# Kernel optimization log

Hardware: AMD Instinct MI355X
Metric: run time of the kernel (lower is better)

## Reference

```python
import jax, jax.numpy as jnp
import numpy as np

TEMPERATURE = 10.0  # module init temperature (training mode)


def setup_inputs() -> dict:
    key = jax.random.key(0)
    kx, kg = jax.random.split(key)
    B, C, H, W = 64, 128, 64, 64
    n = C * H * W  # 524288
    x = jax.random.normal(kx, (B, C, H, W), dtype=jnp.float32)
    # Gumbel(0,1) noise for Gumbel-top-k sampling (== multinomial w/o replacement)
    u = jax.random.uniform(kg, (B, n), dtype=jnp.float32, minval=1e-20, maxval=1.0)
    gumbel = -jnp.log(-jnp.log(u))
    k = int(round(0.1 * n))  # percent_on * n = 52429
    return {"x": x, "gumbel": gumbel, "k": k}


def reference(x, gumbel, k):
    B = x.shape[0]
    n = x.shape[1] * x.shape[2] * x.shape[3]
    flat = x.reshape(B, n)                      # [B, n]
    logits = flat / TEMPERATURE
    # Categorical sampling of k winners without replacement == top-k of
    # gumbel-perturbed logits (equivalent to softmax(logits) + multinomial).
    _, idx = jax.lax.top_k(logits + gumbel, k)  # [B, k]
    mask = jnp.zeros((B, n), dtype=x.dtype).at[jnp.arange(B)[:, None], idx].set(1.0)
    out = (flat * mask).reshape(x.shape)
    return jnp.maximum(out, 0.0)  # relu=True
```

## Files before the change

kernel.cpp:

```cpp
#include <hip/hip_runtime.h>
#include <cstdint>

#define BROWS 64
#define NCOL  524288
#define CHUNKS 64
#define CHUNK  (NCOL / CHUNKS)
#define NV4    (CHUNK / 4)
#define LCAP   1024
#define ECAP   512
#define MAXCAP 24576
#define M_SAMP 32768
#define SEGS   128
#define SBLK   16
#define SLACK  5200
#define HB2    32768

typedef float nf4 __attribute__((ext_vector_type(4)));

#define ABV_OFF   0u
#define CCNT_OFF  256u
#define RINFO_OFF 512u
#define HIST_OFF  4096u
#define CAND_OFF  4096u
#define ZWORDS    (1024 + BROWS * HB2)

__device__ __forceinline__ uint32_t fkey(float s) {
  uint32_t b = __float_as_uint(s);
  return (b & 0x80000000u) ? ~b : (b | 0x80000000u);
}

__global__ __launch_bounds__(256) void k_zero(uint32_t* __restrict__ p, int n) {
  int i = blockIdx.x * 256 + threadIdx.x;
  if (i < n) p[i] = 0;
}

__global__ __launch_bounds__(256) void k_sampleA(const float* __restrict__ x,
                                                 const float* __restrict__ g,
                                                 uint32_t* __restrict__ hist) {
  int row = blockIdx.y;
  size_t rb = (size_t)row * NCOL;
  uint32_t* gh = hist + (size_t)row * HB2;
  int i0 = blockIdx.x * (M_SAMP / SBLK);
  for (int it = 0; it < (M_SAMP / SBLK) / 256; ++it) {
    int i = i0 + it * 256 + threadIdx.x;
    size_t off = rb + (size_t)(i >> 8) * (NCOL / SEGS) + (i & 255);
    uint32_t key = fkey(x[off] / 10.0f + g[off]);
    atomicAdd(&gh[key >> 17], 1u);
  }
}

__global__ __launch_bounds__(1024) void k_pick(const uint32_t* __restrict__ hist,
                                               const int* __restrict__ kptr,
                                               uint32_t* __restrict__ rinfo,
                                               uint32_t* __restrict__ abv,
                                               uint32_t* __restrict__ ccnt) {
  __shared__ uint32_t part[1024];
  __shared__ uint32_t segbuf[32];
  __shared__ uint32_t sel[4];
  int row = blockIdx.x;
  if (threadIdx.x == 0) { abv[row] = 0; ccnt[row] = 0; }
  const uint32_t* gh = hist + (size_t)row * HB2;
  const uint4* gh4 = (const uint4*)gh;
  uint32_t s = 0;
  #pragma unroll
  for (int j = 0; j < 8; ++j) {
    uint4 v = gh4[threadIdx.x * 8 + j];
    s += v.x + v.y + v.z + v.w;
  }
  part[threadIdx.x] = s;
  __syncthreads();
  if (threadIdx.x == 0) {
    uint32_t kk = (uint32_t)(*kptr);
    uint32_t rHi = ((kk > SLACK ? kk - SLACK : 0u) / 16u) + 1u;
    uint32_t rLo = ((kk + SLACK) / 16u) + 1u;
    if (rLo > M_SAMP) rLo = M_SAMP;
    uint32_t cum = 0, cumHi = 0, cumLo = 0;
    int segHi = -1, segLo = -1;
    for (int t = 1023; t >= 0; --t) {
      uint32_t c = part[t];
      if (segHi < 0 && cum + c >= rHi) { segHi = t; cumHi = cum; }
      if (segLo < 0 && cum + c >= rLo) { segLo = t; cumLo = cum; break; }
      cum += c;
    }
    if (segHi < 0) segHi = 0;
    if (segLo < 0) segLo = 0;
    sel[0] = (uint32_t)segHi; sel[1] = rHi - cumHi;
    sel[2] = (uint32_t)segLo; sel[3] = rLo - cumLo;
  }
  __syncthreads();
  int segHi = (int)sel[0], segLo = (int)sel[2];
  if (threadIdx.x < 32) segbuf[threadIdx.x] = gh[segHi * 32 + threadIdx.x];
  __syncthreads();
  if (threadIdx.x == 0) {
    uint32_t rem = sel[1], cum = 0;
    int bin = 0;
    for (int b = 31; b >= 0; --b) {
      uint32_t c = segbuf[b];
      if (cum + c >= rem) { bin = b; break; }
      cum += c;
    }
    uint32_t binHi = (uint32_t)(segHi * 32 + bin);
    rinfo[row * 4 + 0] = (binHi << 17) | 0x1FFFFu;
  }
  __syncthreads();
  if (threadIdx.x < 32) segbuf[threadIdx.x] = gh[segLo * 32 + threadIdx.x];
  __syncthreads();
  if (threadIdx.x == 0) {
    uint32_t rem = sel[3], cum = 0;
    int bin = 0;
    for (int b = 31; b >= 0; --b) {
      uint32_t c = segbuf[b];
      if (cum + c >= rem) { bin = b; break; }
      cum += c;
    }
    uint32_t binLo = (uint32_t)(segLo * 32 + bin);
    rinfo[row * 4 + 1] = binLo << 17;
  }
}

__global__ __launch_bounds__(256) void k_main(const float* __restrict__ x,
                                              const float* __restrict__ g,
                                              const uint32_t* __restrict__ rinfo,
                                              uint64_t* __restrict__ cand,
                                              float* __restrict__ cval,
                                              uint32_t* __restrict__ ccnt,
                                              uint32_t* __restrict__ abv,
                                              float* __restrict__ out, int cap) {
  __shared__ uint64_t lbuf[LCAP];
  __shared__ float lval[LCAP];
  __shared__ uint32_t lcnt, lbase;
  __shared__ uint32_t wsum[4];
  int row = blockIdx.y, chunk = blockIdx.x;
  uint32_t keyHi = rinfo[row * 4 + 0];
  uint32_t keyLo = rinfo[row * 4 + 1];
  if (threadIdx.x == 0) lcnt = 0;
  __syncthreads();
  size_t base = (size_t)row * NCOL + (size_t)chunk * CHUNK;
  const float4* x4 = (const float4*)(x + base);
  const float4* g4 = (const float4*)(g + base);
  nf4* o4 = (nf4*)(out + base);
  uint32_t mycnt = 0;
  for (int i = threadIdx.x; i < NV4; i += 256) {
    float4 a = x4[i];
    float4 b = g4[i];
    uint32_t f0 = fkey(a.x / 10.0f + b.x);
    uint32_t f1 = fkey(a.y / 10.0f + b.y);
    uint32_t f2 = fkey(a.z / 10.0f + b.z);
    uint32_t f3 = fkey(a.w / 10.0f + b.w);
    nf4 o;
    o.x = (f0 > keyHi) ? fmaxf(a.x, 0.0f) : 0.0f;
    o.y = (f1 > keyHi) ? fmaxf(a.y, 0.0f) : 0.0f;
    o.z = (f2 > keyHi) ? fmaxf(a.z, 0.0f) : 0.0f;
    o.w = (f3 > keyHi) ? fmaxf(a.w, 0.0f) : 0.0f;
    __builtin_nontemporal_store(o, &o4[i]);
    mycnt += (f0 > keyHi) + (f1 > keyHi) + (f2 > keyHi) + (f3 > keyHi);
    uint32_t li = (uint32_t)(chunk * CHUNK + i * 4);
    if (f0 >= keyLo && f0 <= keyHi) { uint32_t p = atomicAdd(&lcnt, 1u); if (p < LCAP) { lbuf[p] = ((uint64_t)f0 << 32) | li;        lval[p] = fmaxf(a.x, 0.0f); } }
    if (f1 >= keyLo && f1 <= keyHi) { uint32_t p = atomicAdd(&lcnt, 1u); if (p < LCAP) { lbuf[p] = ((uint64_t)f1 << 32) | (li + 1u); lval[p] = fmaxf(a.y, 0.0f); } }
    if (f2 >= keyLo && f2 <= keyHi) { uint32_t p = atomicAdd(&lcnt, 1u); if (p < LCAP) { lbuf[p] = ((uint64_t)f2 << 32) | (li + 2u); lval[p] = fmaxf(a.z, 0.0f); } }
    if (f3 >= keyLo && f3 <= keyHi) { uint32_t p = atomicAdd(&lcnt, 1u); if (p < LCAP) { lbuf[p] = ((uint64_t)f3 << 32) | (li + 3u); lval[p] = fmaxf(a.w, 0.0f); } }
  }
  for (int off = 32; off > 0; off >>= 1) mycnt += __shfl_down(mycnt, off);
  int lane = threadIdx.x & 63, wid = threadIdx.x >> 6;
  if (lane == 0) wsum[wid] = mycnt;
  __syncthreads();
  if (threadIdx.x == 0) {
    atomicAdd(&abv[row], wsum[0] + wsum[1] + wsum[2] + wsum[3]);
    lbase = atomicAdd(&ccnt[row], lcnt < LCAP ? lcnt : (uint32_t)LCAP);
  }
  __syncthreads();
  uint32_t cnt = lcnt < LCAP ? lcnt : (uint32_t)LCAP;
  uint64_t* dst = cand + (size_t)row * (size_t)cap;
  float* dv = cval + (size_t)row * (size_t)cap;
  for (uint32_t i = threadIdx.x; i < cnt; i += 256) {
    uint32_t p = lbase + i;
    if (p < (uint32_t)cap) { dst[p] = lbuf[i]; dv[p] = lval[i]; }
  }
}

__global__ __launch_bounds__(256) void k_finalize(const float* __restrict__ x,
                                                  const uint64_t* __restrict__ cand,
                                                  const float* __restrict__ cval,
                                                  const uint32_t* __restrict__ ccnt,
                                                  const uint32_t* __restrict__ abv,
                                                  const uint32_t* __restrict__ rinfo,
                                                  const int* __restrict__ kptr,
                                                  float* __restrict__ out, int cap) {
  __shared__ uint32_t h[4096];
  __shared__ uint32_t part[256];
  __shared__ uint64_t elist[ECAP];
  __shared__ uint32_t ecnt;
  __shared__ int s_cut, s_need2;
  int row = blockIdx.x;
  uint32_t m = ccnt[row];
  if (m > (uint32_t)cap) m = (uint32_t)cap;
  int need = (int)((uint32_t)(*kptr)) - (int)abv[row];
  if (need <= 0) return;
  size_t rb = (size_t)row * NCOL;
  const uint64_t* c = cand + (size_t)row * (size_t)cap;
  const float* cv = cval + (size_t)row * (size_t)cap;
  if ((uint32_t)need >= m) {
    for (uint32_t i = threadIdx.x; i < m; i += 256) {
      uint32_t idx = (uint32_t)c[i];
      out[rb + idx] = cv[i];
    }
    return;
  }
  uint32_t keyLo = rinfo[row * 4 + 1];
  uint32_t range = rinfo[row * 4 + 0] - keyLo;
  int bits = 32 - __clz((int)(range | 1u));
  int shift = bits > 12 ? bits - 12 : 0;
  for (int i = threadIdx.x; i < 4096; i += 256) h[i] = 0;
  if (threadIdx.x == 0) ecnt = 0;
  __syncthreads();
  for (uint32_t i = threadIdx.x; i < m; i += 256) {
    uint32_t key = (uint32_t)(c[i] >> 32);
    atomicAdd(&h[(key - keyLo) >> shift], 1u);
  }
  __syncthreads();
  uint32_t s = 0;
  for (int j = 0; j < 16; ++j) s += h[threadIdx.x * 16 + j];
  part[threadIdx.x] = s;
  __syncthreads();
  if (threadIdx.x == 0) {
    uint32_t cum = 0;
    int seg = 255;
    for (; seg > 0; --seg) {
      if (cum + part[seg] >= (uint32_t)need) break;
      cum += part[seg];
    }
    int bin = seg * 16 + 15;
    for (; bin > seg * 16; --bin) {
      if (cum + h[bin] >= (uint32_t)need) break;
      cum += h[bin];
    }
    s_cut = bin;
    s_need2 = need - (int)cum;
  }
  __syncthreads();
  int cut = s_cut, need2 = s_need2;
  for (uint32_t i = threadIdx.x; i < m; i += 256) {
    uint64_t e = c[i];
    int bin = (int)(((uint32_t)(e >> 32) - keyLo) >> shift);
    if (bin > cut) {
      out[rb + (uint32_t)e] = cv[i];
    } else if (bin == cut) {
      uint32_t p = atomicAdd(&ecnt, 1u);
      if (p < ECAP) elist[p] = e ^ 0xFFFFFFFFull;
    }
  }
  __syncthreads();
  int mm = (int)(ecnt < (uint32_t)ECAP ? ecnt : (uint32_t)ECAP);
  for (int pass = 0; pass < mm; ++pass) {
    for (int i = threadIdx.x; 2 * i + (pass & 1) + 1 < mm; i += 256) {
      int a2 = 2 * i + (pass & 1);
      uint64_t va = elist[a2], vb = elist[a2 + 1];
      if (vb > va) { elist[a2] = vb; elist[a2 + 1] = va; }
    }
    __syncthreads();
  }
  int w = need2 < mm ? need2 : mm;
  for (int i = threadIdx.x; i < w; i += 256) {
    uint32_t idx = ~(uint32_t)elist[i];
    out[rb + idx] = fmaxf(x[rb + idx], 0.0f);
  }
}

extern "C" void kernel_launch(void* const* d_in, const int* in_sizes, int n_in,
                              void* d_out, int out_size, void* d_ws, size_t ws_size,
                              hipStream_t stream) {
  const float* x = (const float*)d_in[0];
  const float* g = (const float*)d_in[1];
  const int* kptr = (const int*)d_in[2];
  float* out = (float*)d_out;
  char* ws = (char*)d_ws;

  uint32_t* abv = (uint32_t*)(ws + ABV_OFF);
  uint32_t* ccnt = (uint32_t*)(ws + CCNT_OFF);
  uint32_t* rinfo = (uint32_t*)(ws + RINFO_OFF);
  uint32_t* hist = (uint32_t*)(ws + HIST_OFF);
  uint64_t* cand = (uint64_t*)(ws + CAND_OFF);

  long cap_avail = ((long)ws_size - (long)CAND_OFF) / (12 * BROWS);
  int cap = cap_avail < MAXCAP ? (int)cap_avail : MAXCAP;
  if (cap < 1) cap = 1;
  float* cval = (float*)(ws + CAND_OFF + (size_t)BROWS * (size_t)cap * 8u);

  k_zero<<<(ZWORDS + 255) / 256, 256, 0, stream>>>((uint32_t*)ws, ZWORDS);
  dim3 sgrid(SBLK, BROWS);
  k_sampleA<<<sgrid, 256, 0, stream>>>(x, g, hist);
  k_pick<<<BROWS, 1024, 0, stream>>>(hist, kptr, rinfo, abv, ccnt);
  dim3 grid(CHUNKS, BROWS);
  k_main<<<grid, 256, 0, stream>>>(x, g, rinfo, cand, cval, ccnt, abv, out, cap);
  k_finalize<<<BROWS, 256, 0, stream>>>(x, cand, cval, ccnt, abv, rinfo, kptr, out, cap);
}
```

Before: 214.5 us.

## Coarsen sample histogram, batch candidate atomics, split finalize into cut and scatter

The sample histogram drops from 32768 to 16384 bins per row, so there is less to zero and scan, and it uses twice as many sample blocks. Candidate appends in the main pass now take one shared atomic per float4 group instead of one per element. The old per-row finalize kernel is split in two: a 64-block cut kernel picks the boundary bin and handles ties, and a separate 16x64-block scatter kernel writes the candidates above the cut, giving more parallelism for the scattered writes. The trade-offs are an extra kernel launch and a wider candidate key window, which could leave more candidates per row.

```diff
diff --git a/kernel.cpp b/kernel.cpp
--- a/kernel.cpp
+++ b/kernel.cpp
@@ -11,9 +11,10 @@
 #define MAXCAP 24576
 #define M_SAMP 32768
 #define SEGS   128
-#define SBLK   16
+#define SBLK   32
 #define SLACK  5200
-#define HB2    32768
+#define HB2    16384
+#define NSCAT  16
 
 typedef float nf4 __attribute__((ext_vector_type(4)));
 
@@ -45,7 +46,7 @@
     int i = i0 + it * 256 + threadIdx.x;
     size_t off = rb + (size_t)(i >> 8) * (NCOL / SEGS) + (i & 255);
     uint32_t key = fkey(x[off] / 10.0f + g[off]);
-    atomicAdd(&gh[key >> 17], 1u);
+    atomicAdd(&gh[key >> 18], 1u);
   }
 }
 
@@ -55,7 +56,7 @@
                                                uint32_t* __restrict__ abv,
                                                uint32_t* __restrict__ ccnt) {
   __shared__ uint32_t part[1024];
-  __shared__ uint32_t segbuf[32];
+  __shared__ uint32_t segbuf[16];
   __shared__ uint32_t sel[4];
   int row = blockIdx.x;
   if (threadIdx.x == 0) { abv[row] = 0; ccnt[row] = 0; }
@@ -63,8 +64,8 @@
   const uint4* gh4 = (const uint4*)gh;
   uint32_t s = 0;
   #pragma unroll
-  for (int j = 0; j < 8; ++j) {
-    uint4 v = gh4[threadIdx.x * 8 + j];
+  for (int j = 0; j < 4; ++j) {
+    uint4 v = gh4[threadIdx.x * 4 + j];
     s += v.x + v.y + v.z + v.w;
   }
   part[threadIdx.x] = s;
@@ -89,32 +90,32 @@
   }
   __syncthreads();
   int segHi = (int)sel[0], segLo = (int)sel[2];
-  if (threadIdx.x < 32) segbuf[threadIdx.x] = gh[segHi * 32 + threadIdx.x];
+  if (threadIdx.x < 16) segbuf[threadIdx.x] = gh[segHi * 16 + threadIdx.x];
   __syncthreads();
   if (threadIdx.x == 0) {
     uint32_t rem = sel[1], cum = 0;
     int bin = 0;
-    for (int b = 31; b >= 0; --b) {
+    for (int b = 15; b >= 0; --b) {
       uint32_t c = segbuf[b];
       if (cum + c >= rem) { bin = b; break; }
       cum += c;
     }
-    uint32_t binHi = (uint32_t)(segHi * 32 + bin);
-    rinfo[row * 4 + 0] = (binHi << 17) | 0x1FFFFu;
-  }
-  __syncthreads();
-  if (threadIdx.x < 32) segbuf[threadIdx.x] = gh[segLo * 32 + threadIdx.x];
+    uint32_t binHi = (uint32_t)(segHi * 16 + bin);
+    rinfo[row * 4 + 0] = (binHi << 18) | 0x3FFFFu;
+  }
+  __syncthreads();
+  if (threadIdx.x < 16) segbuf[threadIdx.x] = gh[segLo * 16 + threadIdx.x];
   __syncthreads();
   if (threadIdx.x == 0) {
     uint32_t rem = sel[3], cum = 0;
     int bin = 0;
-    for (int b = 31; b >= 0; --b) {
+    for (int b = 15; b >= 0; --b) {
       uint32_t c = segbuf[b];
       if (cum + c >= rem) { bin = b; break; }
       cum += c;
     }
-    uint32_t binLo = (uint32_t)(segLo * 32 + bin);
-    rinfo[row * 4 + 1] = binLo << 17;
+    uint32_t binLo = (uint32_t)(segLo * 16 + bin);
+    rinfo[row * 4 + 1] = binLo << 18;
   }
 }
 
@@ -154,11 +155,19 @@
     o.w = (f3 > keyHi) ? fmaxf(a.w, 0.0f) : 0.0f;
     __builtin_nontemporal_store(o, &o4[i]);
     mycnt += (f0 > keyHi) + (f1 > keyHi) + (f2 > keyHi) + (f3 > keyHi);
-    uint32_t li = (uint32_t)(chunk * CHUNK + i * 4);
-    if (f0 >= keyLo && f0 <= keyHi) { uint32_t p = atomicAdd(&lcnt, 1u); if (p < LCAP) { lbuf[p] = ((uint64_t)f0 << 32) | li;        lval[p] = fmaxf(a.x, 0.0f); } }
-    if (f1 >= keyLo && f1 <= keyHi) { uint32_t p = atomicAdd(&lcnt, 1u); if (p < LCAP) { lbuf[p] = ((uint64_t)f1 << 32) | (li + 1u); lval[p] = fmaxf(a.y, 0.0f); } }
-    if (f2 >= keyLo && f2 <= keyHi) { uint32_t p = atomicAdd(&lcnt, 1u); if (p < LCAP) { lbuf[p] = ((uint64_t)f2 << 32) | (li + 2u); lval[p] = fmaxf(a.z, 0.0f); } }
-    if (f3 >= keyLo && f3 <= keyHi) { uint32_t p = atomicAdd(&lcnt, 1u); if (p < LCAP) { lbuf[p] = ((uint64_t)f3 << 32) | (li + 3u); lval[p] = fmaxf(a.w, 0.0f); } }
+    bool c0 = (f0 >= keyLo) && (f0 <= keyHi);
+    bool c1 = (f1 >= keyLo) && (f1 <= keyHi);
+    bool c2 = (f2 >= keyLo) && (f2 <= keyHi);
+    bool c3 = (f3 >= keyLo) && (f3 <= keyHi);
+    uint32_t nh = (uint32_t)c0 + (uint32_t)c1 + (uint32_t)c2 + (uint32_t)c3;
+    if (nh) {
+      uint32_t li = (uint32_t)(chunk * CHUNK + i * 4);
+      uint32_t p = atomicAdd(&lcnt, nh);
+      if (c0) { if (p < LCAP) { lbuf[p] = ((uint64_t)f0 << 32) | li;        lval[p] = fmaxf(a.x, 0.0f); } p++; }
+      if (c1) { if (p < LCAP) { lbuf[p] = ((uint64_t)f1 << 32) | (li + 1u); lval[p] = fmaxf(a.y, 0.0f); } p++; }
+      if (c2) { if (p < LCAP) { lbuf[p] = ((uint64_t)f2 << 32) | (li + 2u); lval[p] = fmaxf(a.z, 0.0f); } p++; }
+      if (c3) { if (p < LCAP) { lbuf[p] = ((uint64_t)f3 << 32) | (li + 3u); lval[p] = fmaxf(a.w, 0.0f); } p++; }
+    }
   }
   for (int off = 32; off > 0; off >>= 1) mycnt += __shfl_down(mycnt, off);
   int lane = threadIdx.x & 63, wid = threadIdx.x >> 6;
@@ -178,14 +187,13 @@
   }
 }
 
-__global__ __launch_bounds__(256) void k_finalize(const float* __restrict__ x,
-                                                  const uint64_t* __restrict__ cand,
-                                                  const float* __restrict__ cval,
-                                                  const uint32_t* __restrict__ ccnt,
-                                                  const uint32_t* __restrict__ abv,
-                                                  const uint32_t* __restrict__ rinfo,
-                                                  const int* __restrict__ kptr,
-                                                  float* __restrict__ out, int cap) {
+__global__ __launch_bounds__(256) void k_cut(const float* __restrict__ x,
+                                             const uint64_t* __restrict__ cand,
+                                             const uint32_t* __restrict__ ccnt,
+                                             const uint32_t* __restrict__ abv,
+                                             uint32_t* __restrict__ rinfo,
+                                             const int* __restrict__ kptr,
+                                             float* __restrict__ out, int cap) {
   __shared__ uint32_t h[4096];
   __shared__ uint32_t part[256];
   __shared__ uint64_t elist[ECAP];
@@ -195,17 +203,10 @@
   uint32_t m = ccnt[row];
   if (m > (uint32_t)cap) m = (uint32_t)cap;
   int need = (int)((uint32_t)(*kptr)) - (int)abv[row];
-  if (need <= 0) return;
+  if (need <= 0) { if (threadIdx.x == 0) rinfo[row * 4 + 2] = 0x7FFFFFFFu; return; }
+  if ((uint32_t)need >= m) { if (threadIdx.x == 0) rinfo[row * 4 + 2] = (uint32_t)(-1); return; }
   size_t rb = (size_t)row * NCOL;
   const uint64_t* c = cand + (size_t)row * (size_t)cap;
-  const float* cv = cval + (size_t)row * (size_t)cap;
-  if ((uint32_t)need >= m) {
-    for (uint32_t i = threadIdx.x; i < m; i += 256) {
-      uint32_t idx = (uint32_t)c[i];
-      out[rb + idx] = cv[i];
-    }
-    return;
-  }
   uint32_t keyLo = rinfo[row * 4 + 1];
   uint32_t range = rinfo[row * 4 + 0] - keyLo;
   int bits = 32 - __clz((int)(range | 1u));
@@ -236,15 +237,14 @@
     }
     s_cut = bin;
     s_need2 = need - (int)cum;
+    rinfo[row * 4 + 2] = (uint32_t)bin;
   }
   __syncthreads();
   int cut = s_cut, need2 = s_need2;
   for (uint32_t i = threadIdx.x; i < m; i += 256) {
     uint64_t e = c[i];
     int bin = (int)(((uint32_t)(e >> 32) - keyLo) >> shift);
-    if (bin > cut) {
-      out[rb + (uint32_t)e] = cv[i];
-    } else if (bin == cut) {
+    if (bin == cut) {
       uint32_t p = atomicAdd(&ecnt, 1u);
       if (p < ECAP) elist[p] = e ^ 0xFFFFFFFFull;
     }
@@ -263,6 +263,33 @@
   for (int i = threadIdx.x; i < w; i += 256) {
     uint32_t idx = ~(uint32_t)elist[i];
     out[rb + idx] = fmaxf(x[rb + idx], 0.0f);
+  }
+}
+
+__global__ __launch_bounds__(256) void k_scatter(const uint64_t* __restrict__ cand,
+                                                 const float* __restrict__ cval,
+                                                 const uint32_t* __restrict__ ccnt,
+                                                 const uint32_t* __restrict__ rinfo,
+                                                 float* __restrict__ out, int cap) {
+  int row = blockIdx.y;
+  uint32_t m = ccnt[row];
+  if (m > (uint32_t)cap) m = (uint32_t)cap;
+  int cut = (int)rinfo[row * 4 + 2];
+  if (cut == 0x7FFFFFFF) return;
+  uint32_t keyLo = rinfo[row * 4 + 1];
+  uint32_t range = rinfo[row * 4 + 0] - keyLo;
+  int bits = 32 - __clz((int)(range | 1u));
+  int shift = bits > 12 ? bits - 12 : 0;
+  size_t rb = (size_t)row * NCOL;
+  const uint64_t* c = cand + (size_t)row * (size_t)cap;
+  const float* cv = cval + (size_t)row * (size_t)cap;
+  uint32_t slice = (m + NSCAT - 1) / NSCAT;
+  uint32_t i0 = blockIdx.x * slice;
+  uint32_t i1 = i0 + slice < m ? i0 + slice : m;
+  for (uint32_t i = i0 + threadIdx.x; i < i1; i += 256) {
+    uint64_t e = c[i];
+    int bin = (int)(((uint32_t)(e >> 32) - keyLo) >> shift);
+    if (bin > cut) out[rb + (uint32_t)e] = cv[i];
   }
 }
 
@@ -292,5 +319,7 @@
   k_pick<<<BROWS, 1024, 0, stream>>>(hist, kptr, rinfo, abv, ccnt);
   dim3 grid(CHUNKS, BROWS);
   k_main<<<grid, 256, 0, stream>>>(x, g, rinfo, cand, cval, ccnt, abv, out, cap);
-  k_finalize<<<BROWS, 256, 0, stream>>>(x, cand, cval, ccnt, abv, rinfo, kptr, out, cap);
-}
+  k_cut<<<BROWS, 256, 0, stream>>>(x, cand, ccnt, abv, rinfo, kptr, out, cap);
+  dim3 scgrid(NSCAT, BROWS);
+  k_scatter<<<scgrid, 256, 0, stream>>>(cand, cval, ccnt, rinfo, out, cap);
+}
```

Result: slower. 221.7 us (+3.4%).
